# Optimization experiments

Measured on AMD Instinct MI355X. Metric: run time of the kernel, lower is better.

## Reference

```python
import jax, jax.numpy as jnp
import numpy as np

B, T, D = 32, 256, 1024      # batch, seq_len, input_size
H = D // 2                   # LSTM hidden size = 512
K = 128                      # num_tags


def setup_inputs() -> dict:
    key = jax.random.key(0)
    ks = jax.random.split(key, 16)
    s_in = 1.0 / np.sqrt(D + K)
    s_h = 1.0 / np.sqrt(H)
    return {
        "hiddens": jax.random.normal(ks[0], (B, T, D), jnp.float32),
        "h_t": jax.random.normal(ks[1], (2, B, H), jnp.float32),
        "c_t": jax.random.normal(ks[2], (2, B, H), jnp.float32),
        "mask": jnp.ones((B, T), jnp.float32),
        # output layer: Linear(H, K)
        "W_out": jax.random.normal(ks[3], (K, H), jnp.float32) * s_h,
        "b_out": jnp.zeros((K,), jnp.float32),
        # LSTM layer 0: input dim = K + D
        "W_ih0": jax.random.normal(ks[4], (4 * H, K + D), jnp.float32) * s_in,
        "W_hh0": jax.random.normal(ks[5], (4 * H, H), jnp.float32) * s_h,
        "b_ih0": jnp.zeros((4 * H,), jnp.float32),
        "b_hh0": jnp.zeros((4 * H,), jnp.float32),
        # LSTM layer 1: input dim = H
        "W_ih1": jax.random.normal(ks[6], (4 * H, H), jnp.float32) * s_h,
        "W_hh1": jax.random.normal(ks[7], (4 * H, H), jnp.float32) * s_h,
        "b_ih1": jnp.zeros((4 * H,), jnp.float32),
        "b_hh1": jnp.zeros((4 * H,), jnp.float32),
    }


def _lstm_cell(x, h, c, W_ih, W_hh, b_ih, b_hh):
    g = x @ W_ih.T + h @ W_hh.T + b_ih + b_hh
    i, f, gg, o = jnp.split(g, 4, axis=-1)
    i = jax.nn.sigmoid(i); f = jax.nn.sigmoid(f)
    gg = jnp.tanh(gg); o = jax.nn.sigmoid(o)
    c = f * c + i * gg
    h = o * jnp.tanh(c)
    return h, c


def reference(hiddens, h_t, c_t, mask, W_out, b_out,
              W_ih0, W_hh0, b_ih0, b_hh0, W_ih1, W_hh1, b_ih1, b_hh1):
    # initial previous-tag distribution from first frame's first half
    last_tag = hiddens[:, 0, :H] @ W_out.T + b_out          # [B,K]
    sm = jax.nn.softmax(last_tag, axis=-1)

    def step(carry, x_t):
        h1, c1, h2, c2, sm = carry
        inp = jnp.concatenate([x_t, sm], axis=-1)           # [B, D+K]
        h1, c1 = _lstm_cell(inp, h1, c1, W_ih0, W_hh0, b_ih0, b_hh0)
        h2, c2 = _lstm_cell(h1, h2, c2, W_ih1, W_hh1, b_ih1, b_hh1)
        logit = h2 @ W_out.T + b_out                        # [B,K]
        sm = jax.nn.softmax(logit, axis=-1)
        return (h1, c1, h2, c2, sm), logit

    carry0 = (h_t[0], c_t[0], h_t[1], c_t[1], sm)
    _, logits_t = jax.lax.scan(step, carry0, jnp.swapaxes(hiddens, 0, 1))  # [T,B,K]
    logits = jnp.swapaxes(logits_t, 0, 1)                   # [B,T,K]
    logits = logits + (1.0 - mask)[:, :, None] * jnp.float32(-1e32)
    prob = jax.nn.softmax(logits, axis=-1)
    return prob
```

## Files before the change

### kernel.cpp

```cpp
#include <hip/hip_runtime.h>
#include <cstdint>
#include <cstddef>


#define Bz   32
#define Tz   256
#define Dz   1024
#define Hz   512
#define NK   128
#define IN0  1152
#define NBLK 256
#define BH   16384

typedef float vf4 __attribute__((ext_vector_type(4)));

__device__ __forceinline__ void ldsc4(vf4& d, const float* p) {
  asm volatile("global_load_dwordx4 %0, %1, off sc0 sc1" : "=v"(d) : "v"(p));
}
__device__ __forceinline__ void ldg1(float& d, const float* p) {
  asm volatile("global_load_dword %0, %1, off" : "=v"(d) : "v"(p));
}
__device__ __forceinline__ void stsc1(float* p, float v) {
  asm volatile("global_store_dword %0, %1, off sc0 sc1" :: "v"(p), "v"(v) : "memory");
}
__device__ __forceinline__ void stsc1u(unsigned int* p, unsigned int v) {
  asm volatile("global_store_dword %0, %1, off sc0 sc1" :: "v"(p), "v"(v) : "memory");
}
#define FENCE8(c, a0,a1,a2,a3,a4,a5,a6,a7) \
  asm volatile("s_waitcnt vmcnt(" #c ")" : "+v"(a0),"+v"(a1),"+v"(a2),"+v"(a3), \
               "+v"(a4),"+v"(a5),"+v"(a6),"+v"(a7) :: "memory")

#define FMA4(acc, W_, A_) \
  acc = fmaf((W_).x,(A_).x, fmaf((W_).y,(A_).y, fmaf((W_).z,(A_).z, fmaf((W_).w,(A_).w,(acc)))))

__device__ __forceinline__ float sigf(float x) { return 1.0f / (1.0f + expf(-x)); }

__device__ __forceinline__ void gbar(unsigned int* slots, unsigned int* bcast,
                                     int gidx, bool master, unsigned int g) {
  asm volatile("s_waitcnt vmcnt(0)" ::: "memory");
  __syncthreads();
  if (threadIdx.x == 0)
    __hip_atomic_store(slots + gidx * 16, g,
                       __ATOMIC_RELAXED, __HIP_MEMORY_SCOPE_SYSTEM);
  if (master) {
    if (threadIdx.x < 128) {
      unsigned int* wsl = slots + threadIdx.x * 16;
      while (__hip_atomic_load(wsl, __ATOMIC_RELAXED, __HIP_MEMORY_SCOPE_SYSTEM) < g)
        __builtin_amdgcn_s_sleep(1);
    }
    __syncthreads();
    if (threadIdx.x == 0) {
      asm volatile("s_waitcnt vmcnt(0)" ::: "memory");
      __hip_atomic_store(bcast, g, __ATOMIC_RELAXED, __HIP_MEMORY_SCOPE_SYSTEM);
    }
  } else if (threadIdx.x == 0) {
    while (__hip_atomic_load(bcast, __ATOMIC_RELAXED, __HIP_MEMORY_SCOPE_SYSTEM) < g)
      __builtin_amdgcn_s_sleep(1);
  }
  __syncthreads();
}

__device__ __forceinline__ void garrive(unsigned int* slots, int gidx,
                                        unsigned int g) {
  asm volatile("s_waitcnt vmcnt(0)" ::: "memory");
  __syncthreads();
  if (threadIdx.x == 0)
    __hip_atomic_store(slots + gidx * 16, g,
                       __ATOMIC_RELAXED, __HIP_MEMORY_SCOPE_SYSTEM);
}

#define FMAROW(r, AV, BASE, KOFF) \
  { vf4 wv = *(const vf4*)&BASE[r][KOFF]; FMA4(A##r, wv, AV); }
#define R16A(OP, AV, BASE, KOFF) \
  OP(0,AV,BASE,KOFF) OP(1,AV,BASE,KOFF) OP(2,AV,BASE,KOFF) OP(3,AV,BASE,KOFF) \
  OP(4,AV,BASE,KOFF) OP(5,AV,BASE,KOFF) OP(6,AV,BASE,KOFF) OP(7,AV,BASE,KOFF) \
  OP(8,AV,BASE,KOFF) OP(9,AV,BASE,KOFF) OP(10,AV,BASE,KOFF) OP(11,AV,BASE,KOFF) \
  OP(12,AV,BASE,KOFF) OP(13,AV,BASE,KOFF) OP(14,AV,BASE,KOFF) OP(15,AV,BASE,KOFF)

#define RED16 { \
  { const bool hi = (ks & 1) != 0; \
    float s0=hi?A0:A8, s1=hi?A1:A9, s2=hi?A2:A10, s3=hi?A3:A11; \
    float s4=hi?A4:A12, s5=hi?A5:A13, s6=hi?A6:A14, s7=hi?A7:A15; \
    float k0=hi?A8:A0, k1=hi?A9:A1, k2=hi?A10:A2, k3=hi?A11:A3; \
    float k4=hi?A12:A4, k5=hi?A13:A5, k6=hi?A14:A6, k7=hi?A15:A7; \
    A0=k0+__shfl_xor(s0,1,64); A1=k1+__shfl_xor(s1,1,64); \
    A2=k2+__shfl_xor(s2,1,64); A3=k3+__shfl_xor(s3,1,64); \
    A4=k4+__shfl_xor(s4,1,64); A5=k5+__shfl_xor(s5,1,64); \
    A6=k6+__shfl_xor(s6,1,64); A7=k7+__shfl_xor(s7,1,64); } \
  { const bool hi = (ks & 2) != 0; \
    float s0=hi?A0:A4, s1=hi?A1:A5, s2=hi?A2:A6, s3=hi?A3:A7; \
    float k0=hi?A4:A0, k1=hi?A5:A1, k2=hi?A6:A2, k3=hi?A7:A3; \
    A0=k0+__shfl_xor(s0,2,64); A1=k1+__shfl_xor(s1,2,64); \
    A2=k2+__shfl_xor(s2,2,64); A3=k3+__shfl_xor(s3,2,64); } \
  { const bool hi = (ks & 4) != 0; \
    float s0=hi?A0:A2, s1=hi?A1:A3; float k0=hi?A2:A0, k1=hi?A3:A1; \
    A0=k0+__shfl_xor(s0,4,64); A1=k1+__shfl_xor(s1,4,64); } \
  { const bool hi = (ks & 8) != 0; \
    float s0=hi?A0:A1; float k0=hi?A1:A0; \
    A0=k0+__shfl_xor(s0,8,64); } }

#define ZERO16 A0=0.f;A1=0.f;A2=0.f;A3=0.f;A4=0.f;A5=0.f;A6=0.f;A7=0.f; \
               A8=0.f;A9=0.f;A10=0.f;A11=0.f;A12=0.f;A13=0.f;A14=0.f;A15=0.f;

#define GATES(CREG, HDST) \
  __syncthreads(); \
  if (tid < 64) { \
    float gi = gbuf[cu][cbl],      gf = gbuf[4 + cu][cbl]; \
    float gg = gbuf[8 + cu][cbl],  go = gbuf[12 + cu][cbl]; \
    CREG = sigf(gf) * CREG + sigf(gi) * tanhf(gg); \
    stsc1(HDST + (size_t)(pg * 16 + cbl) * Hz + jg * 4 + cu, \
          sigf(go) * tanhf(CREG)); \
  }

__device__ void c_slot(const float* src, int t, int bb,
                       const float* __restrict__ W_out, const float* __restrict__ b_out,
                       const float* __restrict__ mask,
                       float* __restrict__ smg, float* __restrict__ out,
                       float (*cpart)[2], float* wred,
                       unsigned int* smflag, unsigned int fval) {
  const int tid = threadIdx.x;
  const int n = tid & 127, kh = tid >> 7;
  float p = 0.0f;
  const float* w  = W_out + (size_t)n * Hz + kh * 256;
  const float* s2 = src + kh * 256;
  #pragma unroll 8
  for (int k = 0; k < 256; k += 4) {
    vf4 sv = *(const vf4*)(s2 + k);
    vf4 wv = *(const vf4*)(w + k);
    p += sv.x * wv.x + sv.y * wv.y + sv.z * wv.z + sv.w * wv.w;
  }
  cpart[n][kh] = p;
  __syncthreads();
  float logit = 0.0f;
  if (tid < 128) logit = cpart[n][0] + cpart[n][1] + b_out[n];
  float m = logit;
  #pragma unroll
  for (int off = 32; off >= 1; off >>= 1) m = fmaxf(m, __shfl_xor(m, off));
  if ((tid & 63) == 0 && tid < 128) wred[tid >> 6] = m;
  __syncthreads();
  float M = fmaxf(wred[0], wred[1]);
  float e = (tid < 128) ? expf(logit - M) : 0.0f;
  float s = e;
  #pragma unroll
  for (int off = 32; off >= 1; off >>= 1) s += __shfl_xor(s, off);
  if ((tid & 63) == 0 && tid < 128) wred[2 + (tid >> 6)] = s;
  __syncthreads();
  float S = wred[2] + wred[3];
  if (tid < 128) stsc1(smg + bb * NK + n, e / S);
  asm volatile("s_waitcnt vmcnt(0)" ::: "memory");
  __syncthreads();
  if (fval && tid == 0) stsc1u(smflag, fval);
  if (t >= 0) {
    float mk = (tid < 128) ? mask[bb * Tz + t] : 1.0f;
    float lm = (tid < 128) ? (logit + (1.0f - mk) * (-1e32f)) : -3.0e38f;
    float m2 = lm;
    #pragma unroll
    for (int off = 32; off >= 1; off >>= 1) m2 = fmaxf(m2, __shfl_xor(m2, off));
    if ((tid & 63) == 0 && tid < 128) wred[4 + (tid >> 6)] = m2;
    __syncthreads();
    float M2 = fmaxf(wred[4], wred[5]);
    float e2 = (tid < 128) ? expf(lm - M2) : 0.0f;
    float s2r = e2;
    #pragma unroll
    for (int off = 32; off >= 1; off >>= 1) s2r += __shfl_xor(s2r, off);
    if ((tid & 63) == 0 && tid < 128) wred[6 + (tid >> 6)] = s2r;
    __syncthreads();
    float S2 = wred[6] + wred[7];
    if (tid < 128) out[((size_t)bb * Tz + t) * NK + n] = e2 / S2;
  }
}

__global__ void __launch_bounds__(256)
xpre_kernel(const float* __restrict__ hiddens, const float* __restrict__ W_ih0,
            const float* __restrict__ b_ih0, const float* __restrict__ b_hh0,
            float* __restrict__ Xpre, int t0, int colTiles, int cstride) {
  __shared__ float Ws[16][64];
  __shared__ float Hs[16][64];
  const int tid = threadIdx.x;
  const int bx = blockIdx.x % colTiles;
  const int by = blockIdx.x / colTiles;
  const int n0 = by * 64, c0 = bx * 64;
  const int tx = tid & 15, ty = tid >> 4;
  const int ldn = tid >> 2;
  const int ldk = (tid & 3) * 4;

  const int bb = ldn & 31;
  const int tt = t0 + (c0 >> 5) + (ldn >> 5);
  const float* hsrc = hiddens + ((size_t)bb * Tz + tt) * Dz + ldk;
  const float* wsrc = W_ih0 + (size_t)(n0 + ldn) * IN0 + ldk;

  float acc[4][4] = {};
  vf4 wv = *(const vf4*)(wsrc);
  vf4 hv = *(const vf4*)(hsrc);
  for (int k0 = 0; k0 < Dz; k0 += 16) {
    __syncthreads();
    Ws[ldk + 0][ldn] = wv.x; Ws[ldk + 1][ldn] = wv.y;
    Ws[ldk + 2][ldn] = wv.z; Ws[ldk + 3][ldn] = wv.w;
    Hs[ldk + 0][ldn] = hv.x; Hs[ldk + 1][ldn] = hv.y;
    Hs[ldk + 2][ldn] = hv.z; Hs[ldk + 3][ldn] = hv.w;
    __syncthreads();
    if (k0 + 16 < Dz) {
      wv = *(const vf4*)(wsrc + k0 + 16);
      hv = *(const vf4*)(hsrc + k0 + 16);
    }
    #pragma unroll
    for (int k = 0; k < 16; ++k) {
      vf4 a4 = *(const vf4*)&Ws[k][ty * 4];
      vf4 b4 = *(const vf4*)&Hs[k][tx * 4];
      acc[0][0] += a4.x * b4.x; acc[0][1] += a4.x * b4.y; acc[0][2] += a4.x * b4.z; acc[0][3] += a4.x * b4.w;
      acc[1][0] += a4.y * b4.x; acc[1][1] += a4.y * b4.y; acc[1][2] += a4.y * b4.z; acc[1][3] += a4.y * b4.w;
      acc[2][0] += a4.z * b4.x; acc[2][1] += a4.z * b4.y; acc[2][2] += a4.z * b4.z; acc[2][3] += a4.z * b4.w;
      acc[3][0] += a4.w * b4.x; acc[3][1] += a4.w * b4.y; acc[3][2] += a4.w * b4.z; acc[3][3] += a4.w * b4.w;
    }
  }
  #pragma unroll
  for (int i = 0; i < 4; ++i) {
    int n = n0 + ty * 4 + i;
    float bi = b_ih0[n] + b_hh0[n];
    vf4 v; v.x = acc[i][0] + bi; v.y = acc[i][1] + bi;
    v.z = acc[i][2] + bi; v.w = acc[i][3] + bi;
    *(vf4*)(Xpre + (size_t)n * cstride + c0 + tx * 4) = v;
  }
}

__global__ void __launch_bounds__(256)
seq_kernel(const float* __restrict__ hiddens,
           const float* __restrict__ h_t, const float* __restrict__ c_t,
           const float* __restrict__ mask,
           const float* __restrict__ W_out, const float* __restrict__ b_out,
           const float* __restrict__ W_ih0, const float* __restrict__ W_hh0,
           const float* __restrict__ W_ih1, const float* __restrict__ W_hh1,
           const float* __restrict__ b_ih1, const float* __restrict__ b_hh1,
           const float* __restrict__ Xpre, float* __restrict__ out,
           float* __restrict__ h1g, float* __restrict__ h2g,
           float* __restrict__ smg, float* __restrict__ c1g, float* __restrict__ c2g,
           unsigned int* bar, int t0, int nsteps, int cstride) {
  __shared__ float wA[16][640];
  __shared__ float wB[16][1024];
  __shared__ float gbuf[16][17];
  __shared__ float biasB[16];
  __shared__ float hsg[512];
  __shared__ float cpart[128][2];
  __shared__ float wred[8];

  const int tid = threadIdx.x;
  const int bid = blockIdx.x;
  const int jg  = bid >> 1;
  const int pg  = bid & 1;
  const int ks  = tid & 15;
  const int bbl = tid >> 4;
  const int bbg = pg * 16 + bbl;
  const int ks4 = ks * 4;
  const int cu  = tid & 3, cbl = tid >> 2;
  const int rr  = ((ks & 1) << 3) | ((ks & 2) << 1) | ((ks & 4) >> 1) | ((ks & 8) >> 3);
  const int rowG = ((rr >> 2) * Hz) + jg * 4 + (rr & 3);
  const int hb = ((bid & 1) << 4) | (bid >> 1);

  unsigned int* barg = bar + pg * 2048;
  unsigned int* bcst = bar + 4096 + pg * 16;
  unsigned int* smf  = bar + 4608;
  const int  gidx    = bid >> 1;
  const bool gmaster = (gidx == 127);

  #pragma clang loop unroll(disable)
  for (int r = 0; r < 16; ++r) {
    const int row = ((r >> 2) * Hz) + jg * 4 + (r & 3);
    if (tid * 4 < 512)
      *(vf4*)&wA[r][tid * 4] = *(const vf4*)(W_hh0 + (size_t)row * Hz + tid * 4);
    if (tid * 4 < 128)
      *(vf4*)&wA[r][512 + tid * 4] = *(const vf4*)(W_ih0 + (size_t)row * IN0 + 1024 + tid * 4);
    if (tid * 4 < 512) {
      *(vf4*)&wB[r][tid * 4]       = *(const vf4*)(W_ih1 + (size_t)row * Hz + tid * 4);
      *(vf4*)&wB[r][512 + tid * 4] = *(const vf4*)(W_hh1 + (size_t)row * Hz + tid * 4);
    }
  }
  if (tid < 16) {
    const int row = ((tid >> 2) * Hz) + jg * 4 + (tid & 3);
    biasB[tid] = b_ih1[row] + b_hh1[row];
  }

  float c1r = 0.0f, c2r = 0.0f;
  if (tid < 64) {
    const size_t ci = (size_t)(pg * 16 + cbl) * Hz + jg * 4 + cu;
    if (t0 == 0) { c1r = c_t[ci]; c2r = c_t[BH + ci]; }
    else         { c1r = c1g[ci]; c2r = c2g[ci]; }
  }

  if (t0 == 0) {
    if (bid < 32 && tid < 128) {
      vf4 v1 = *(const vf4*)(h_t + (size_t)hb * Hz + tid * 4);
      vf4 v2 = *(const vf4*)(h_t + BH + (size_t)hb * Hz + tid * 4);
      float* d1 = h1g + BH + (size_t)hb * Hz + tid * 4;
      float* d2 = h2g + BH + (size_t)hb * Hz + tid * 4;
      stsc1(d1, v1.x); stsc1(d1 + 1, v1.y); stsc1(d1 + 2, v1.z); stsc1(d1 + 3, v1.w);
      stsc1(d2, v2.x); stsc1(d2 + 1, v2.y); stsc1(d2 + 2, v2.z); stsc1(d2 + 3, v2.w);
    }
    if (bid < 32) {
      if (tid < 128)
        *(vf4*)&hsg[tid * 4] = *(const vf4*)(hiddens + (size_t)hb * Tz * Dz + tid * 4);
      __syncthreads();
      c_slot(hsg, -1, hb, W_out, b_out, mask, smg, out, cpart, wred,
             smf + hb * 16, 0u);
    }
  }
  __syncthreads();
  unsigned int g = 1;
  gbar(barg, bcst, gidx, gmaster, g); ++g;

  #pragma clang loop unroll(disable)
  for (int k = 0; k < nsteps; ++k) {
    const int t = t0 + k;
    const float* h1prev = h1g + ((t + 1) & 1) * BH;
    float*       h1cur  = h1g + (t & 1) * BH;
    const float* h2prev = h2g + ((t + 1) & 1) * BH;
    float*       h2cur  = h2g + (t & 1) * BH;
    float A0,A1,A2,A3,A4,A5,A6,A7,A8,A9,A10,A11,A12,A13,A14,A15;

    {
      vf4 ah0,ah1,ah2,ah3,ah4,ah5,ah6,ah7, as0,as1;
      const float* hp = h1prev + (size_t)bbg * Hz + ks4;
      ldsc4(ah0, hp);        ldsc4(ah1, hp + 64);  ldsc4(ah2, hp + 128);
      ldsc4(ah3, hp + 192);  ldsc4(ah4, hp + 256); ldsc4(ah5, hp + 320);
      ldsc4(ah6, hp + 384);  ldsc4(ah7, hp + 448);
      float xv;
      ldg1(xv, Xpre + (size_t)rowG * cstride + k * 32 + bbg);
      ZERO16
      FENCE8(1, ah0,ah1,ah2,ah3,ah4,ah5,ah6,ah7);
      R16A(FMAROW, ah0, wA, ks4 +   0)
      R16A(FMAROW, ah1, wA, ks4 +  64)
      R16A(FMAROW, ah2, wA, ks4 + 128)
      R16A(FMAROW, ah3, wA, ks4 + 192)
      R16A(FMAROW, ah4, wA, ks4 + 256)
      R16A(FMAROW, ah5, wA, ks4 + 320)
      R16A(FMAROW, ah6, wA, ks4 + 384)
      R16A(FMAROW, ah7, wA, ks4 + 448)
      RED16
      const float partA = A0;
      if (k > 0) {
        const unsigned int tgt = (unsigned int)k;
        if (tid < 16) {
          const unsigned int* fp = smf + (pg * 16 + tid) * 16;
          while (__hip_atomic_load(fp, __ATOMIC_RELAXED,
                                   __HIP_MEMORY_SCOPE_SYSTEM) < tgt)
            __builtin_amdgcn_s_sleep(1);
        }
        __syncthreads();
      }
      const float* sp = smg + (size_t)bbg * NK + ks4;
      ldsc4(as0, sp);        ldsc4(as1, sp + 64);
      ZERO16
      asm volatile("s_waitcnt vmcnt(0)" : "+v"(as0), "+v"(as1), "+v"(xv) :: "memory");
      R16A(FMAROW, as0, wA, ks4 + 512)
      R16A(FMAROW, as1, wA, ks4 + 576)
      RED16
      gbuf[rr][bbl] = partA + A0 + xv;
      GATES(c1r, h1cur)
    }
    gbar(barg, bcst, gidx, gmaster, g); ++g;

    {
      vf4 aa0,aa1,aa2,aa3,aa4,aa5,aa6,aa7, ab0,ab1,ab2,ab3,ab4,ab5,ab6,ab7;
      const float* p1 = h1cur + (size_t)bbg * Hz + ks4;
      ldsc4(aa0, p1);       ldsc4(aa1, p1 + 64);  ldsc4(aa2, p1 + 128);
      ldsc4(aa3, p1 + 192); ldsc4(aa4, p1 + 256); ldsc4(aa5, p1 + 320);
      ldsc4(aa6, p1 + 384); ldsc4(aa7, p1 + 448);
      const float* p2 = h2prev + (size_t)bbg * Hz + ks4;
      ldsc4(ab0, p2);       ldsc4(ab1, p2 + 64);  ldsc4(ab2, p2 + 128);
      ldsc4(ab3, p2 + 192); ldsc4(ab4, p2 + 256); ldsc4(ab5, p2 + 320);
      ldsc4(ab6, p2 + 384); ldsc4(ab7, p2 + 448);
      ZERO16
      FENCE8(8, aa0,aa1,aa2,aa3,aa4,aa5,aa6,aa7);
      R16A(FMAROW, aa0, wB, ks4 +   0)
      R16A(FMAROW, aa1, wB, ks4 +  64)
      R16A(FMAROW, aa2, wB, ks4 + 128)
      R16A(FMAROW, aa3, wB, ks4 + 192)
      R16A(FMAROW, aa4, wB, ks4 + 256)
      R16A(FMAROW, aa5, wB, ks4 + 320)
      R16A(FMAROW, aa6, wB, ks4 + 384)
      R16A(FMAROW, aa7, wB, ks4 + 448)
      FENCE8(0, ab0,ab1,ab2,ab3,ab4,ab5,ab6,ab7);
      R16A(FMAROW, ab0, wB, ks4 + 512)
      R16A(FMAROW, ab1, wB, ks4 + 576)
      R16A(FMAROW, ab2, wB, ks4 + 640)
      R16A(FMAROW, ab3, wB, ks4 + 704)
      R16A(FMAROW, ab4, wB, ks4 + 768)
      R16A(FMAROW, ab5, wB, ks4 + 832)
      R16A(FMAROW, ab6, wB, ks4 + 896)
      R16A(FMAROW, ab7, wB, ks4 + 960)
      RED16
      gbuf[rr][bbl] = A0 + biasB[rr];
      GATES(c2r, h2cur)
    }
    const unsigned int gP2 = g;
    garrive(barg, gidx, gP2); ++g;

    if (bid < 32) {
      if (tid < 128) {
        unsigned int* wsl = barg + tid * 16;
        while (__hip_atomic_load(wsl, __ATOMIC_RELAXED,
                                 __HIP_MEMORY_SCOPE_SYSTEM) < gP2)
          __builtin_amdgcn_s_sleep(1);
      }
      __syncthreads();
      if (tid < 128) {
        vf4 v;
        ldsc4(v, h2cur + (size_t)hb * Hz + tid * 4);
        asm volatile("s_waitcnt vmcnt(0)" : "+v"(v) :: "memory");
        *(vf4*)&hsg[tid * 4] = v;
      }
      __syncthreads();
      c_slot(hsg, t, hb, W_out, b_out, mask, smg, out, cpart, wred,
             smf + hb * 16, (unsigned int)(k + 1));
    }
  }

  if (tid < 64) {
    const size_t ci = (size_t)(pg * 16 + cbl) * Hz + jg * 4 + cu;
    stsc1(c1g + ci, c1r);
    stsc1(c2g + ci, c2r);
  }
}

extern "C" void kernel_launch(void* const* d_in, const int* in_sizes, int n_in,
                              void* d_out, int out_size, void* d_ws, size_t ws_size,
                              hipStream_t stream) {
  (void)in_sizes; (void)n_in; (void)out_size;
  const float* hiddens = (const float*)d_in[0];
  const float* h_t     = (const float*)d_in[1];
  const float* c_t     = (const float*)d_in[2];
  const float* mask    = (const float*)d_in[3];
  const float* W_out   = (const float*)d_in[4];
  const float* b_out   = (const float*)d_in[5];
  const float* W_ih0   = (const float*)d_in[6];
  const float* W_hh0   = (const float*)d_in[7];
  const float* b_ih0   = (const float*)d_in[8];
  const float* b_hh0   = (const float*)d_in[9];
  const float* W_ih1   = (const float*)d_in[10];
  const float* W_hh1   = (const float*)d_in[11];
  const float* b_ih1   = (const float*)d_in[12];
  const float* b_hh1   = (const float*)d_in[13];
  float* out = (float*)d_out;

  unsigned int* bar = (unsigned int*)d_ws;
  float* base = (float*)((char*)d_ws + 32768);
  float* h1g  = base;
  float* h2g  = h1g + 2 * BH;
  float* smg  = h2g + 2 * BH;
  float* c1g  = smg + Bz * NK;
  float* c2g  = c1g + BH;
  float* Xpre = c2g + BH;

  const size_t fullNeed = 32768 + (size_t)(102400 + 2048 * 8192) * 4;
  const bool full = ws_size >= fullNeed;
  const int NCH    = full ? 1 : 16;
  const int CH     = full ? Tz : 16;
  const int cstr   = full ? (Tz * 32) : (16 * 32);
  const int cTiles = cstr / 64;

  for (int c = 0; c < NCH; ++c) {
    const int t0 = c * CH;
    hipMemsetAsync(bar, 0, 32768, stream);
    hipLaunchKernelGGL(xpre_kernel, dim3(32 * cTiles), dim3(256), 0, stream,
                       hiddens, W_ih0, b_ih0, b_hh0, Xpre, t0, cTiles, cstr);
    int nsteps = CH, cs = cstr, tt0 = t0;
    void* ka[] = { (void*)&hiddens, (void*)&h_t, (void*)&c_t, (void*)&mask,
                   (void*)&W_out, (void*)&b_out, (void*)&W_ih0, (void*)&W_hh0,
                   (void*)&W_ih1, (void*)&W_hh1, (void*)&b_ih1, (void*)&b_hh1,
                   (void*)&Xpre, (void*)&out, (void*)&h1g, (void*)&h2g,
                   (void*)&smg, (void*)&c1g, (void*)&c2g, (void*)&bar,
                   (void*)&tt0, (void*)&nsteps, (void*)&cs };
    hipError_t err = hipLaunchCooperativeKernel((void*)seq_kernel, dim3(NBLK),
                                                dim3(256), ka, 0, stream);
    if (err != hipSuccess) {
      hipLaunchKernelGGL(seq_kernel, dim3(NBLK), dim3(256), 0, stream,
                         hiddens, h_t, c_t, mask, W_out, b_out, W_ih0, W_hh0,
                         W_ih1, W_hh1, b_ih1, b_hh1, Xpre, out,
                         h1g, h2g, smg, c1g, c2g, bar, tt0, nsteps, cs);
    }
  }
}
```

Baseline: 5.787 ms.

## Split grid barrier to overlap layer-1 recurrent matvec and defer output softmax

Replaces the full grid barrier after layer 0 with an arrive, then has each block compute the h2prev·W_hh1 half of layer 1 before waiting for the barrier and loading h1cur. The masked output softmax is split out of the critical head and run one step later, in the slack after the arrive. The aim is to hide barrier latency and take the output softmax off the sequential critical path. It adds an lgsave buffer and a trailing epilogue call, and reorders the accumulation order of the layer-1 sum.

```diff
diff --git a/kernel.cpp b/kernel.cpp
--- a/kernel.cpp
+++ b/kernel.cpp
@@ -112,12 +112,12 @@
           sigf(go) * tanhf(CREG)); \
   }
 
-__device__ void c_slot(const float* src, int t, int bb,
-                       const float* __restrict__ W_out, const float* __restrict__ b_out,
-                       const float* __restrict__ mask,
-                       float* __restrict__ smg, float* __restrict__ out,
-                       float (*cpart)[2], float* wred,
-                       unsigned int* smflag, unsigned int fval) {
+__device__ void c_head_crit(const float* src, int bb,
+                            const float* __restrict__ W_out,
+                            const float* __restrict__ b_out,
+                            float* __restrict__ smg,
+                            float (*cpart)[2], float* wred, float* lgsave,
+                            unsigned int* smflag, unsigned int fval) {
   const int tid = threadIdx.x;
   const int n = tid & 127, kh = tid >> 7;
   float p = 0.0f;
@@ -132,7 +132,7 @@
   cpart[n][kh] = p;
   __syncthreads();
   float logit = 0.0f;
-  if (tid < 128) logit = cpart[n][0] + cpart[n][1] + b_out[n];
+  if (tid < 128) { logit = cpart[n][0] + cpart[n][1] + b_out[n]; lgsave[n] = logit; }
   float m = logit;
   #pragma unroll
   for (int off = 32; off >= 1; off >>= 1) m = fmaxf(m, __shfl_xor(m, off));
@@ -150,24 +150,29 @@
   asm volatile("s_waitcnt vmcnt(0)" ::: "memory");
   __syncthreads();
   if (fval && tid == 0) stsc1u(smflag, fval);
-  if (t >= 0) {
-    float mk = (tid < 128) ? mask[bb * Tz + t] : 1.0f;
-    float lm = (tid < 128) ? (logit + (1.0f - mk) * (-1e32f)) : -3.0e38f;
-    float m2 = lm;
-    #pragma unroll
-    for (int off = 32; off >= 1; off >>= 1) m2 = fmaxf(m2, __shfl_xor(m2, off));
-    if ((tid & 63) == 0 && tid < 128) wred[4 + (tid >> 6)] = m2;
-    __syncthreads();
-    float M2 = fmaxf(wred[4], wred[5]);
-    float e2 = (tid < 128) ? expf(lm - M2) : 0.0f;
-    float s2r = e2;
-    #pragma unroll
-    for (int off = 32; off >= 1; off >>= 1) s2r += __shfl_xor(s2r, off);
-    if ((tid & 63) == 0 && tid < 128) wred[6 + (tid >> 6)] = s2r;
-    __syncthreads();
-    float S2 = wred[6] + wred[7];
-    if (tid < 128) out[((size_t)bb * Tz + t) * NK + n] = e2 / S2;
-  }
+}
+
+__device__ void c_head_out(int t, int bb, const float* __restrict__ mask,
+                           float* __restrict__ out,
+                           const float* lgsave, float* wred) {
+  const int tid = threadIdx.x;
+  const int n = tid & 127;
+  float mk = (tid < 128) ? mask[bb * Tz + t] : 1.0f;
+  float lm = (tid < 128) ? (lgsave[n] + (1.0f - mk) * (-1e32f)) : -3.0e38f;
+  float m2 = lm;
+  #pragma unroll
+  for (int off = 32; off >= 1; off >>= 1) m2 = fmaxf(m2, __shfl_xor(m2, off));
+  if ((tid & 63) == 0 && tid < 128) wred[4 + (tid >> 6)] = m2;
+  __syncthreads();
+  float M2 = fmaxf(wred[4], wred[5]);
+  float e2 = (tid < 128) ? expf(lm - M2) : 0.0f;
+  float s2r = e2;
+  #pragma unroll
+  for (int off = 32; off >= 1; off >>= 1) s2r += __shfl_xor(s2r, off);
+  if ((tid & 63) == 0 && tid < 128) wred[6 + (tid >> 6)] = s2r;
+  __syncthreads();
+  float S2 = wred[6] + wred[7];
+  if (tid < 128) out[((size_t)bb * Tz + t) * NK + n] = e2 / S2;
 }
 
 __global__ void __launch_bounds__(256)
@@ -242,6 +247,7 @@
   __shared__ float hsg[512];
   __shared__ float cpart[128][2];
   __shared__ float wred[8];
+  __shared__ float lgsave[128];
 
   const int tid = threadIdx.x;
   const int bid = blockIdx.x;
@@ -299,8 +305,8 @@
       if (tid < 128)
         *(vf4*)&hsg[tid * 4] = *(const vf4*)(hiddens + (size_t)hb * Tz * Dz + tid * 4);
       __syncthreads();
-      c_slot(hsg, -1, hb, W_out, b_out, mask, smg, out, cpart, wred,
-             smf + hb * 16, 0u);
+      c_head_crit(hsg, hb, W_out, b_out, smg, cpart, wred, lgsave,
+                  smf + hb * 16, 0u);
     }
   }
   __syncthreads();
@@ -356,28 +362,19 @@
       gbuf[rr][bbl] = partA + A0 + xv;
       GATES(c1r, h1cur)
     }
-    gbar(barg, bcst, gidx, gmaster, g); ++g;
+    const unsigned int gA = g;
+    garrive(barg, gidx, gA); ++g;
+
+    if (bid < 32 && k > 0)
+      c_head_out(t - 1, hb, mask, out, lgsave, wred);
 
     {
-      vf4 aa0,aa1,aa2,aa3,aa4,aa5,aa6,aa7, ab0,ab1,ab2,ab3,ab4,ab5,ab6,ab7;
-      const float* p1 = h1cur + (size_t)bbg * Hz + ks4;
-      ldsc4(aa0, p1);       ldsc4(aa1, p1 + 64);  ldsc4(aa2, p1 + 128);
-      ldsc4(aa3, p1 + 192); ldsc4(aa4, p1 + 256); ldsc4(aa5, p1 + 320);
-      ldsc4(aa6, p1 + 384); ldsc4(aa7, p1 + 448);
+      vf4 ab0,ab1,ab2,ab3,ab4,ab5,ab6,ab7;
       const float* p2 = h2prev + (size_t)bbg * Hz + ks4;
       ldsc4(ab0, p2);       ldsc4(ab1, p2 + 64);  ldsc4(ab2, p2 + 128);
       ldsc4(ab3, p2 + 192); ldsc4(ab4, p2 + 256); ldsc4(ab5, p2 + 320);
       ldsc4(ab6, p2 + 384); ldsc4(ab7, p2 + 448);
       ZERO16
-      FENCE8(8, aa0,aa1,aa2,aa3,aa4,aa5,aa6,aa7);
-      R16A(FMAROW, aa0, wB, ks4 +   0)
-      R16A(FMAROW, aa1, wB, ks4 +  64)
-      R16A(FMAROW, aa2, wB, ks4 + 128)
-      R16A(FMAROW, aa3, wB, ks4 + 192)
-      R16A(FMAROW, aa4, wB, ks4 + 256)
-      R16A(FMAROW, aa5, wB, ks4 + 320)
-      R16A(FMAROW, aa6, wB, ks4 + 384)
-      R16A(FMAROW, aa7, wB, ks4 + 448)
       FENCE8(0, ab0,ab1,ab2,ab3,ab4,ab5,ab6,ab7);
       R16A(FMAROW, ab0, wB, ks4 + 512)
       R16A(FMAROW, ab1, wB, ks4 + 576)
@@ -387,18 +384,48 @@
       R16A(FMAROW, ab5, wB, ks4 + 832)
       R16A(FMAROW, ab6, wB, ks4 + 896)
       R16A(FMAROW, ab7, wB, ks4 + 960)
+      if (gmaster) {
+        if (tid < 128) {
+          unsigned int* wsl = barg + tid * 16;
+          while (__hip_atomic_load(wsl, __ATOMIC_RELAXED,
+                                   __HIP_MEMORY_SCOPE_SYSTEM) < gA)
+            __builtin_amdgcn_s_sleep(1);
+        }
+        __syncthreads();
+        if (tid == 0)
+          __hip_atomic_store(bcst, gA, __ATOMIC_RELAXED, __HIP_MEMORY_SCOPE_SYSTEM);
+      } else if (tid == 0) {
+        while (__hip_atomic_load(bcst, __ATOMIC_RELAXED,
+                                 __HIP_MEMORY_SCOPE_SYSTEM) < gA)
+          __builtin_amdgcn_s_sleep(1);
+      }
+      __syncthreads();
+      vf4 aa0,aa1,aa2,aa3,aa4,aa5,aa6,aa7;
+      const float* p1 = h1cur + (size_t)bbg * Hz + ks4;
+      ldsc4(aa0, p1);       ldsc4(aa1, p1 + 64);  ldsc4(aa2, p1 + 128);
+      ldsc4(aa3, p1 + 192); ldsc4(aa4, p1 + 256); ldsc4(aa5, p1 + 320);
+      ldsc4(aa6, p1 + 384); ldsc4(aa7, p1 + 448);
+      FENCE8(0, aa0,aa1,aa2,aa3,aa4,aa5,aa6,aa7);
+      R16A(FMAROW, aa0, wB, ks4 +   0)
+      R16A(FMAROW, aa1, wB, ks4 +  64)
+      R16A(FMAROW, aa2, wB, ks4 + 128)
+      R16A(FMAROW, aa3, wB, ks4 + 192)
+      R16A(FMAROW, aa4, wB, ks4 + 256)
+      R16A(FMAROW, aa5, wB, ks4 + 320)
+      R16A(FMAROW, aa6, wB, ks4 + 384)
+      R16A(FMAROW, aa7, wB, ks4 + 448)
       RED16
       gbuf[rr][bbl] = A0 + biasB[rr];
       GATES(c2r, h2cur)
     }
-    const unsigned int gP2 = g;
-    garrive(barg, gidx, gP2); ++g;
+    const unsigned int gB = g;
+    garrive(barg, gidx, gB); ++g;
 
     if (bid < 32) {
       if (tid < 128) {
         unsigned int* wsl = barg + tid * 16;
         while (__hip_atomic_load(wsl, __ATOMIC_RELAXED,
-                                 __HIP_MEMORY_SCOPE_SYSTEM) < gP2)
+                                 __HIP_MEMORY_SCOPE_SYSTEM) < gB)
           __builtin_amdgcn_s_sleep(1);
       }
       __syncthreads();
@@ -409,10 +436,13 @@
         *(vf4*)&hsg[tid * 4] = v;
       }
       __syncthreads();
-      c_slot(hsg, t, hb, W_out, b_out, mask, smg, out, cpart, wred,
-             smf + hb * 16, (unsigned int)(k + 1));
-    }
-  }
+      c_head_crit(hsg, hb, W_out, b_out, smg, cpart, wred, lgsave,
+                  smf + hb * 16, (unsigned int)(k + 1));
+    }
+  }
+
+  if (bid < 32)
+    c_head_out(t0 + nsteps - 1, hb, mask, out, lgsave, wred);
 
   if (tid < 64) {
     const size_t ci = (size_t)(pg * 16 + cbl) * Hz + jg * 4 + cu;
```

Result: slower. 7.048 ms (+21.8%).

## Offload masked output softmax from critical head blocks to helper blocks

Applied to the files above, without the earlier changes.

Splits the per-step output head in two. The critical path (logits, softmax feedback, flag) stays on the first 32 blocks. The masked output softmax and the store to out move to blocks 32-63, which run it one step later after their barrier wait. Logits pass between them through a new global buffer, and a final drain step waits on the softmax flag before handling the last timestep. The aim is to shorten the serial chain between steps. In exchange it adds extra global traffic and a dependency on the lagged buffer not being overwritten before it is read.

```diff
diff --git a/kernel.cpp b/kernel.cpp
--- a/kernel.cpp
+++ b/kernel.cpp
@@ -112,12 +112,12 @@
           sigf(go) * tanhf(CREG)); \
   }
 
-__device__ void c_slot(const float* src, int t, int bb,
-                       const float* __restrict__ W_out, const float* __restrict__ b_out,
-                       const float* __restrict__ mask,
-                       float* __restrict__ smg, float* __restrict__ out,
-                       float (*cpart)[2], float* wred,
-                       unsigned int* smflag, unsigned int fval) {
+__device__ void c_head_crit(const float* src, int bb,
+                            const float* __restrict__ W_out,
+                            const float* __restrict__ b_out,
+                            float* __restrict__ smg, float* __restrict__ lggb,
+                            float (*cpart)[2], float* wred,
+                            unsigned int* smflag, unsigned int fval) {
   const int tid = threadIdx.x;
   const int n = tid & 127, kh = tid >> 7;
   float p = 0.0f;
@@ -132,7 +132,10 @@
   cpart[n][kh] = p;
   __syncthreads();
   float logit = 0.0f;
-  if (tid < 128) logit = cpart[n][0] + cpart[n][1] + b_out[n];
+  if (tid < 128) {
+    logit = cpart[n][0] + cpart[n][1] + b_out[n];
+    stsc1(lggb + n, logit);
+  }
   float m = logit;
   #pragma unroll
   for (int off = 32; off >= 1; off >>= 1) m = fmaxf(m, __shfl_xor(m, off));
@@ -150,24 +153,32 @@
   asm volatile("s_waitcnt vmcnt(0)" ::: "memory");
   __syncthreads();
   if (fval && tid == 0) stsc1u(smflag, fval);
-  if (t >= 0) {
-    float mk = (tid < 128) ? mask[bb * Tz + t] : 1.0f;
-    float lm = (tid < 128) ? (logit + (1.0f - mk) * (-1e32f)) : -3.0e38f;
-    float m2 = lm;
-    #pragma unroll
-    for (int off = 32; off >= 1; off >>= 1) m2 = fmaxf(m2, __shfl_xor(m2, off));
-    if ((tid & 63) == 0 && tid < 128) wred[4 + (tid >> 6)] = m2;
-    __syncthreads();
-    float M2 = fmaxf(wred[4], wred[5]);
-    float e2 = (tid < 128) ? expf(lm - M2) : 0.0f;
-    float s2r = e2;
-    #pragma unroll
-    for (int off = 32; off >= 1; off >>= 1) s2r += __shfl_xor(s2r, off);
-    if ((tid & 63) == 0 && tid < 128) wred[6 + (tid >> 6)] = s2r;
-    __syncthreads();
-    float S2 = wred[6] + wred[7];
-    if (tid < 128) out[((size_t)bb * Tz + t) * NK + n] = e2 / S2;
-  }
+}
+
+__device__ void c_head_out(int t, int bb, const float* __restrict__ mask,
+                           float* __restrict__ out,
+                           const float* __restrict__ lggb, float* wred) {
+  const int tid = threadIdx.x;
+  const int n = tid & 127;
+  float lg = 0.0f;
+  if (tid < 128)
+    lg = __hip_atomic_load(lggb + n, __ATOMIC_RELAXED, __HIP_MEMORY_SCOPE_SYSTEM);
+  float mk = (tid < 128) ? mask[bb * Tz + t] : 1.0f;
+  float lm = (tid < 128) ? (lg + (1.0f - mk) * (-1e32f)) : -3.0e38f;
+  float m2 = lm;
+  #pragma unroll
+  for (int off = 32; off >= 1; off >>= 1) m2 = fmaxf(m2, __shfl_xor(m2, off));
+  if ((tid & 63) == 0 && tid < 128) wred[4 + (tid >> 6)] = m2;
+  __syncthreads();
+  float M2 = fmaxf(wred[4], wred[5]);
+  float e2 = (tid < 128) ? expf(lm - M2) : 0.0f;
+  float s2r = e2;
+  #pragma unroll
+  for (int off = 32; off >= 1; off >>= 1) s2r += __shfl_xor(s2r, off);
+  if ((tid & 63) == 0 && tid < 128) wred[6 + (tid >> 6)] = s2r;
+  __syncthreads();
+  float S2 = wred[6] + wred[7];
+  if (tid < 128) out[((size_t)bb * Tz + t) * NK + n] = e2 / S2;
 }
 
 __global__ void __launch_bounds__(256)
@@ -234,6 +245,7 @@
            const float* __restrict__ Xpre, float* __restrict__ out,
            float* __restrict__ h1g, float* __restrict__ h2g,
            float* __restrict__ smg, float* __restrict__ c1g, float* __restrict__ c2g,
+           float* __restrict__ lgg,
            unsigned int* bar, int t0, int nsteps, int cstride) {
   __shared__ float wA[16][640];
   __shared__ float wB[16][1024];
@@ -255,6 +267,8 @@
   const int rr  = ((ks & 1) << 3) | ((ks & 2) << 1) | ((ks & 4) >> 1) | ((ks & 8) >> 3);
   const int rowG = ((rr >> 2) * Hz) + jg * 4 + (rr & 3);
   const int hb = ((bid & 1) << 4) | (bid >> 1);
+  const bool isbud = (bid >= 32 && bid < 64);
+  const int  bb2   = isbud ? (((bid & 1) << 4) | ((bid >> 1) - 16)) : 0;
 
   unsigned int* barg = bar + pg * 2048;
   unsigned int* bcst = bar + 4096 + pg * 16;
@@ -299,8 +313,8 @@
       if (tid < 128)
         *(vf4*)&hsg[tid * 4] = *(const vf4*)(hiddens + (size_t)hb * Tz * Dz + tid * 4);
       __syncthreads();
-      c_slot(hsg, -1, hb, W_out, b_out, mask, smg, out, cpart, wred,
-             smf + hb * 16, 0u);
+      c_head_crit(hsg, hb, W_out, b_out, smg, lgg + hb * NK, cpart, wred,
+                  smf + hb * 16, 0u);
     }
   }
   __syncthreads();
@@ -345,6 +359,8 @@
             __builtin_amdgcn_s_sleep(1);
         }
         __syncthreads();
+        if (isbud)
+          c_head_out(t - 1, bb2, mask, out, lgg + bb2 * NK, wred);
       }
       const float* sp = smg + (size_t)bbg * NK + ks4;
       ldsc4(as0, sp);        ldsc4(as1, sp + 64);
@@ -391,14 +407,14 @@
       gbuf[rr][bbl] = A0 + biasB[rr];
       GATES(c2r, h2cur)
     }
-    const unsigned int gP2 = g;
-    garrive(barg, gidx, gP2); ++g;
+    const unsigned int gB = g;
+    garrive(barg, gidx, gB); ++g;
 
     if (bid < 32) {
       if (tid < 128) {
         unsigned int* wsl = barg + tid * 16;
         while (__hip_atomic_load(wsl, __ATOMIC_RELAXED,
-                                 __HIP_MEMORY_SCOPE_SYSTEM) < gP2)
+                                 __HIP_MEMORY_SCOPE_SYSTEM) < gB)
           __builtin_amdgcn_s_sleep(1);
       }
       __syncthreads();
@@ -409,9 +425,20 @@
         *(vf4*)&hsg[tid * 4] = v;
       }
       __syncthreads();
-      c_slot(hsg, t, hb, W_out, b_out, mask, smg, out, cpart, wred,
-             smf + hb * 16, (unsigned int)(k + 1));
-    }
+      c_head_crit(hsg, hb, W_out, b_out, smg, lgg + hb * NK, cpart, wred,
+                  smf + hb * 16, (unsigned int)(k + 1));
+    }
+  }
+
+  if (isbud) {
+    if (tid == 0) {
+      const unsigned int* fp = smf + bb2 * 16;
+      while (__hip_atomic_load(fp, __ATOMIC_RELAXED,
+                               __HIP_MEMORY_SCOPE_SYSTEM) < (unsigned int)nsteps)
+        __builtin_amdgcn_s_sleep(1);
+    }
+    __syncthreads();
+    c_head_out(t0 + nsteps - 1, bb2, mask, out, lgg + bb2 * NK, wred);
   }
 
   if (tid < 64) {
@@ -448,9 +475,10 @@
   float* smg  = h2g + 2 * BH;
   float* c1g  = smg + Bz * NK;
   float* c2g  = c1g + BH;
-  float* Xpre = c2g + BH;
-
-  const size_t fullNeed = 32768 + (size_t)(102400 + 2048 * 8192) * 4;
+  float* lgg  = c2g + BH;
+  float* Xpre = lgg + Bz * NK;
+
+  const size_t fullNeed = 32768 + (size_t)(102400 + Bz * NK + 2048 * 8192) * 4;
   const bool full = ws_size >= fullNeed;
   const int NCH    = full ? 1 : 16;
   const int CH     = full ? Tz : 16;
@@ -467,15 +495,15 @@
                    (void*)&W_out, (void*)&b_out, (void*)&W_ih0, (void*)&W_hh0,
                    (void*)&W_ih1, (void*)&W_hh1, (void*)&b_ih1, (void*)&b_hh1,
                    (void*)&Xpre, (void*)&out, (void*)&h1g, (void*)&h2g,
-                   (void*)&smg, (void*)&c1g, (void*)&c2g, (void*)&bar,
-                   (void*)&tt0, (void*)&nsteps, (void*)&cs };
+                   (void*)&smg, (void*)&c1g, (void*)&c2g, (void*)&lgg,
+                   (void*)&bar, (void*)&tt0, (void*)&nsteps, (void*)&cs };
     hipError_t err = hipLaunchCooperativeKernel((void*)seq_kernel, dim3(NBLK),
                                                 dim3(256), ka, 0, stream);
     if (err != hipSuccess) {
       hipLaunchKernelGGL(seq_kernel, dim3(NBLK), dim3(256), 0, stream,
                          hiddens, h_t, c_t, mask, W_out, b_out, W_ih0, W_hh0,
                          W_ih1, W_hh1, b_ih1, b_hh1, Xpre, out,
-                         h1g, h2g, smg, c1g, c2g, bar, tt0, nsteps, cs);
-    }
-  }
-}
+                         h1g, h2g, smg, c1g, c2g, lgg, bar, tt0, nsteps, cs);
+    }
+  }
+}
```

Result: no change. 5.735 ms (-0.9%).
